# Performance work log

Measured on AMD Instinct MI355X. Metric: run time of the kernel, lower is better.

## Reference

```python
import jax, jax.numpy as jnp
import numpy as np

B, TE, TD, D = 32, 2048, 64, 1024

def setup_inputs() -> dict:
    key = jax.random.key(0)
    k1, k2, k3, k4, k5 = jax.random.split(key, 5)
    return {
        "encoder_outputs": jax.random.normal(k1, (B, TE, D), dtype=jnp.float32),
        "decoder_outputs": jax.random.normal(k2, (B, TD, D), dtype=jnp.float32),
        "W_a": jax.random.normal(k3, (D, D), dtype=jnp.float32) * (1.0 / np.sqrt(D)),
        "U_a": jax.random.normal(k4, (D, D), dtype=jnp.float32) * (1.0 / np.sqrt(D)),
        "V_a": jax.random.normal(k5, (D, 1), dtype=jnp.float32) * (1.0 / np.sqrt(D)),
    }

def reference(encoder_outputs, decoder_outputs, W_a, U_a, V_a):
    # Bahdanau additive attention over encoder positions, query = last decoder step.
    dec_last = decoder_outputs[:, -1, :]                      # [B, D]
    enc_W = jnp.einsum('bte,ef->btf', encoder_outputs, W_a)   # [B, Te, D]
    dec_U = jnp.einsum('bd,df->bf', dec_last, U_a)            # [B, D] (broadcast over Te instead of tile)
    tanh_out = jnp.tanh(enc_W + dec_U[:, None, :])            # [B, Te, D]
    scores = jnp.einsum('btf,fo->bt', tanh_out, V_a[:, 0:1])  # [B, Te] (squeeze of [B,Te,1])
    weights = jax.nn.softmax(scores, axis=1)                  # [B, Te]
    context = jnp.einsum('bte,bt->be', encoder_outputs, weights)  # [B, D]
    return context, weights[..., None]
```

## Files before the change

kernel.cpp:

```cpp
#include <hip/hip_runtime.h>
#include <stdint.h>

typedef __attribute__((ext_vector_type(8))) __bf16 bf16x8;
typedef __attribute__((ext_vector_type(4))) float  f32x4;

__device__ __forceinline__ uint16_t f2b(float f) {
  uint32_t u = __float_as_uint(f);
  u += 0x7fffu + ((u >> 16) & 1u);
  return (uint16_t)(u >> 16);
}
__device__ __forceinline__ float b2f_lo(uint32_t p) { return __uint_as_float(p << 16); }
__device__ __forceinline__ float b2f_hi(uint32_t p) { return __uint_as_float(p & 0xffff0000u); }

__device__ __forceinline__ float tanh_fast(float x) {
  float e = __expf(2.0f * x);
  return 1.0f - 2.0f / (e + 1.0f);
}

__device__ __forceinline__ void bar() { asm volatile("s_barrier" ::: "memory"); }

__device__ __forceinline__ void gload16(const void* g, void* l) {
  __builtin_amdgcn_global_load_lds(
      (__attribute__((address_space(1))) uint32_t*)g,
      (__attribute__((address_space(3))) uint32_t*)l, 16, 0, 0);
}

__global__ __launch_bounds__(256) void convert_enc(const float4* __restrict__ in,
                                                   uint4* __restrict__ out) {
  int i = blockIdx.x * 256 + threadIdx.x;
  float4 a = in[2 * i], b = in[2 * i + 1];
  uint4 o;
  o.x = (uint32_t)f2b(a.x) | ((uint32_t)f2b(a.y) << 16);
  o.y = (uint32_t)f2b(a.z) | ((uint32_t)f2b(a.w) << 16);
  o.z = (uint32_t)f2b(b.x) | ((uint32_t)f2b(b.y) << 16);
  o.w = (uint32_t)f2b(b.z) | ((uint32_t)f2b(b.w) << 16);
  out[i] = o;
}

__global__ __launch_bounds__(256) void convert_WT(const float* __restrict__ W,
                                                  uint16_t* __restrict__ WT) {
  __shared__ float tile[64][65];
  int k0 = (blockIdx.x & 15) * 64;
  int n0 = (blockIdx.x >> 4) * 64;
  #pragma unroll
  for (int it = 0; it < 16; ++it) {
    int idx = it * 256 + threadIdx.x;
    int kr = idx >> 6, nc = idx & 63;
    tile[kr][nc] = W[(size_t)(k0 + kr) * 1024 + n0 + nc];
  }
  __syncthreads();
  #pragma unroll
  for (int it = 0; it < 16; ++it) {
    int idx = it * 256 + threadIdx.x;
    int nr = idx >> 6, kc = idx & 63;
    WT[(size_t)(n0 + nr) * 1024 + k0 + kc] = f2b(tile[kc][nr]);
  }
}

__global__ __launch_bounds__(256) void compute_u(const float* __restrict__ dec,
                                                 const float4* __restrict__ U4,
                                                 float* __restrict__ u) {
  int b = blockIdx.x >> 3, dseg = blockIdx.x & 7;
  __shared__ float sdec[128];
  if (threadIdx.x < 128)
    sdec[threadIdx.x] = dec[(size_t)b * 64 * 1024 + 63 * 1024 + dseg * 128 + threadIdx.x];
  __syncthreads();
  float4 a = {0.f, 0.f, 0.f, 0.f};
  const float4* Ub = U4 + (size_t)dseg * 128 * 256 + threadIdx.x;
  #pragma unroll 4
  for (int d = 0; d < 128; ++d) {
    float4 w = Ub[(size_t)d * 256];
    float s = sdec[d];
    a.x = fmaf(s, w.x, a.x);
    a.y = fmaf(s, w.y, a.y);
    a.z = fmaf(s, w.z, a.z);
    a.w = fmaf(s, w.w, a.w);
  }
  float* up = u + b * 1024 + threadIdx.x * 4;
  atomicAdd(up + 0, a.x);
  atomicAdd(up + 1, a.y);
  atomicAdd(up + 2, a.z);
  atomicAdd(up + 3, a.w);
}

__global__ __launch_bounds__(512, 2) void gemm_score(const uint16_t* __restrict__ A,
                                                     const uint16_t* __restrict__ BT,
                                                     const float* __restrict__ u,
                                                     const float* __restrict__ v,
                                                     float* __restrict__ spart) {
  __shared__ uint4 lds4[4][2][1024];
  __shared__ float sred[4][256];

  const int bx = blockIdx.x;
  const int wg = (bx & 7) * 128 + (bx >> 3);
  const int mtile = wg >> 2;
  const int ntile = wg & 3;

  const int tid = threadIdx.x;
  const int lane = tid & 63;
  const int wid = tid >> 6;
  const int wr = wid >> 2;
  const int wc = wid & 3;
  const int nib = lane & 15;
  const int q4 = lane >> 4;
  const int fx = q4 ^ ((nib >> 1) & 3);

  const int rowA = mtile * 256;
  const char* baseA = (const char*)A + (size_t)rowA * 2048;
  const char* baseB = (const char*)BT + (size_t)ntile * 256 * 2048;
  const size_t srcoff = (size_t)(tid >> 2) * 2048 +
                        ((size_t)((tid & 3) ^ ((tid >> 3) & 3)) << 4);

#define STAGE_OP(buf, op, srcbase, kt)                                        \
  do {                                                                        \
    const char* _s = (const char*)(srcbase) + (size_t)(kt) * 64;              \
    gload16(_s + srcoff,              &lds4[(buf)][(op)][wid * 64]);          \
    gload16(_s + srcoff + 128 * 2048, &lds4[(buf)][(op)][512 + wid * 64]);    \
  } while (0)

  f32x4 acc[8][4];
  #pragma unroll
  for (int i = 0; i < 8; ++i)
    #pragma unroll
    for (int j = 0; j < 4; ++j) acc[i][j] = (f32x4){0.f, 0.f, 0.f, 0.f};

  STAGE_OP(0, 0, baseA, 0); STAGE_OP(0, 1, baseB, 0);
  STAGE_OP(1, 0, baseA, 1); STAGE_OP(1, 1, baseB, 1);
  STAGE_OP(2, 0, baseA, 2); STAGE_OP(2, 1, baseB, 2);
  asm volatile("s_waitcnt vmcnt(8)" ::: "memory");
  bar();

  bf16x8 bfr[4];

#define PHASE(cb_, qi_, ...)                                                  \
  do {                                                                        \
    bf16x8 af[4];                                                             \
    _Pragma("unroll")                                                         \
    for (int i = 0; i < 4; ++i)                                               \
      af[i] = *(const bf16x8*)&lds4[cb_][0]                                   \
              [(wr * 128 + (qi_) * 64 + i * 16 + nib) * 4 + fx];              \
    if ((qi_) == 0) {                                                         \
      _Pragma("unroll")                                                       \
      for (int j = 0; j < 4; ++j)                                             \
        bfr[j] = *(const bf16x8*)&lds4[cb_][1]                                \
                 [(wc * 64 + j * 16 + nib) * 4 + fx];                         \
    }                                                                         \
    __VA_ARGS__;                                                              \
    bar();                                                                    \
    __builtin_amdgcn_s_setprio(1);                                            \
    _Pragma("unroll")                                                         \
    for (int i = 0; i < 4; ++i)                                               \
      _Pragma("unroll")                                                       \
      for (int j = 0; j < 4; ++j)                                             \
        acc[(qi_) * 4 + i][j] = __builtin_amdgcn_mfma_f32_16x16x32_bf16(      \
            af[i], bfr[j], acc[(qi_) * 4 + i][j], 0, 0, 0);                   \
    __builtin_amdgcn_s_setprio(0);                                            \
  } while (0)

  for (int t = 0; t < 32; ++t) {
    const int cb = t & 3, sb = (t + 3) & 3;
    const bool st = (t < 29);
    PHASE(cb, 0, if (st) STAGE_OP(sb, 0, baseA, t + 3));
    bar();
    PHASE(cb, 1, if (st) STAGE_OP(sb, 1, baseB, t + 3));
    if (t < 29)       asm volatile("s_waitcnt vmcnt(8)" ::: "memory");
    else if (t == 29) asm volatile("s_waitcnt vmcnt(4)" ::: "memory");
    else if (t == 30) asm volatile("s_waitcnt vmcnt(0)" ::: "memory");
    bar();
  }
#undef PHASE
#undef STAGE_OP

  const int b = mtile >> 3;
  float vv[4], uu[4];
  #pragma unroll
  for (int j = 0; j < 4; ++j) {
    int col = ntile * 256 + wc * 64 + j * 16 + nib;
    vv[j] = v[col];
    uu[j] = u[b * 1024 + col];
  }
  #pragma unroll
  for (int qi = 0; qi < 2; ++qi)
    #pragma unroll
    for (int i = 0; i < 4; ++i)
      #pragma unroll
      for (int reg = 0; reg < 4; ++reg) {
        float s = 0.f;
        #pragma unroll
        for (int j = 0; j < 4; ++j) s += vv[j] * tanh_fast(acc[qi * 4 + i][j][reg] + uu[j]);
        s += __shfl_xor(s, 1);
        s += __shfl_xor(s, 2);
        s += __shfl_xor(s, 4);
        s += __shfl_xor(s, 8);
        if (nib == 0) sred[wc][wr * 128 + qi * 64 + i * 16 + q4 * 4 + reg] = s;
      }
  __syncthreads();
  if (tid < 256) {
    float s = sred[0][tid] + sred[1][tid] + sred[2][tid] + sred[3][tid];
    spart[(size_t)ntile * 65536 + rowA + tid] = s;
  }
}

__global__ __launch_bounds__(256) void softmax_k(const float* __restrict__ spart,
                                                 float* __restrict__ wout) {
  int b = blockIdx.x, tid = threadIdx.x;
  __shared__ float red[4];
  float sv[8];
  float mx = -1e30f;
  #pragma unroll
  for (int i = 0; i < 8; ++i) {
    int idx = b * 2048 + i * 256 + tid;
    float s = 0.f;
    #pragma unroll
    for (int j = 0; j < 4; ++j) s += spart[j * 65536 + idx];
    sv[i] = s;
    mx = fmaxf(mx, s);
  }
  #pragma unroll
  for (int off = 1; off < 64; off <<= 1) mx = fmaxf(mx, __shfl_xor(mx, off));
  if ((tid & 63) == 0) red[tid >> 6] = mx;
  __syncthreads();
  mx = fmaxf(fmaxf(red[0], red[1]), fmaxf(red[2], red[3]));
  __syncthreads();
  float sum = 0.f;
  #pragma unroll
  for (int i = 0; i < 8; ++i) {
    sv[i] = __expf(sv[i] - mx);
    sum += sv[i];
  }
  #pragma unroll
  for (int off = 1; off < 64; off <<= 1) sum += __shfl_xor(sum, off);
  if ((tid & 63) == 0) red[tid >> 6] = sum;
  __syncthreads();
  float inv = 1.0f / (red[0] + red[1] + red[2] + red[3]);
  #pragma unroll
  for (int i = 0; i < 8; ++i) wout[b * 2048 + i * 256 + tid] = sv[i] * inv;
}

__global__ __launch_bounds__(256) void context_k(const uint16_t* __restrict__ encA,
                                                 const float* __restrict__ w,
                                                 float* __restrict__ ctx) {
  int b = blockIdx.x >> 4, ch = blockIdx.x & 15;
  int t0 = ch * 128;
  __shared__ float lw[128];
  if (threadIdx.x < 128) lw[threadIdx.x] = w[b * 2048 + t0 + threadIdx.x];
  __syncthreads();
  int th = threadIdx.x >> 7;
  int i  = threadIdx.x & 127;
  int e0 = i * 8;
  float a[8] = {0.f, 0.f, 0.f, 0.f, 0.f, 0.f, 0.f, 0.f};
  const uint16_t* base = encA + (size_t)b * 2048 * 1024 + (size_t)(t0 + th * 64) * 1024 + e0;
  const float* lwp = lw + th * 64;
  #pragma unroll 2
  for (int t = 0; t < 64; ++t) {
    uint4 p = *(const uint4*)(base + (size_t)t * 1024);
    float wt = lwp[t];
    a[0] = fmaf(wt, b2f_lo(p.x), a[0]);
    a[1] = fmaf(wt, b2f_hi(p.x), a[1]);
    a[2] = fmaf(wt, b2f_lo(p.y), a[2]);
    a[3] = fmaf(wt, b2f_hi(p.y), a[3]);
    a[4] = fmaf(wt, b2f_lo(p.z), a[4]);
    a[5] = fmaf(wt, b2f_hi(p.z), a[5]);
    a[6] = fmaf(wt, b2f_lo(p.w), a[6]);
    a[7] = fmaf(wt, b2f_hi(p.w), a[7]);
  }
  float* cp = &ctx[b * 1024 + e0];
  #pragma unroll
  for (int k = 0; k < 8; ++k) atomicAdd(cp + k, a[k]);
}

extern "C" void kernel_launch(void* const* d_in, const int* in_sizes, int n_in,
                              void* d_out, int out_size, void* d_ws, size_t ws_size,
                              hipStream_t stream) {
  const float* enc = (const float*)d_in[0];
  const float* dec = (const float*)d_in[1];
  const float* Wa  = (const float*)d_in[2];
  const float* Ua  = (const float*)d_in[3];
  const float* Va  = (const float*)d_in[4];

  float* out = (float*)d_out;
  float* ctx = out;
  float* wts = out + 32 * 1024;

  char* ws = (char*)d_ws;
  uint16_t* encA  = (uint16_t*)ws;
  uint16_t* WT    = (uint16_t*)(ws + 134217728);
  float*    ub    = (float*)  (ws + 136314880);
  float*    spart = (float*)  (ws + 136445952);

  hipMemsetAsync(ctx, 0, 32 * 1024 * sizeof(float), stream);
  hipMemsetAsync(ub, 0, 32 * 1024 * sizeof(float), stream);

  convert_enc<<<32768, 256, 0, stream>>>((const float4*)enc, (uint4*)encA);
  convert_WT<<<256, 256, 0, stream>>>(Wa, WT);
  compute_u<<<256, 256, 0, stream>>>(dec, (const float4*)Ua, ub);
  gemm_score<<<1024, 512, 0, stream>>>(encA, WT, ub, Va, spart);
  softmax_k<<<32, 256, 0, stream>>>(spart, wts);
  context_k<<<512, 256, 0, stream>>>(encA, wts, ctx);
}
```

Measured before the change: 630.5 us.

## Retile score GEMM to 128x128 with B fragments from global, remove atomics in context

The score GEMM moves from 256x256 tiles with 512 threads and a 4-deep LDS pipeline to 128x128 tiles with 256 threads and 128-wide K steps. Only A is staged in a double-buffered, swizzled LDS, while B fragments are loaded straight from global memory into registers and prefetched one step ahead. Scores are now split across 8 N-tiles, so softmax sums 8 partials. The context kernel writes per-chunk partials that a new reduce kernel sums, replacing float atomics and the memset. The smaller tiles raise global traffic for W and give less reuse per block.

```diff
diff --git a/kernel.cpp b/kernel.cpp
--- a/kernel.cpp
+++ b/kernel.cpp
@@ -18,6 +18,7 @@
 }
 
 __device__ __forceinline__ void bar() { asm volatile("s_barrier" ::: "memory"); }
+__device__ __forceinline__ void cfence() { asm volatile("" ::: "memory"); }
 
 __device__ __forceinline__ void gload16(const void* g, void* l) {
   __builtin_amdgcn_global_load_lds(
@@ -83,121 +84,140 @@
   atomicAdd(up + 3, a.w);
 }
 
-__global__ __launch_bounds__(512, 2) void gemm_score(const uint16_t* __restrict__ A,
+__global__ __launch_bounds__(256, 2) void gemm_score(const uint16_t* __restrict__ A,
                                                      const uint16_t* __restrict__ BT,
                                                      const float* __restrict__ u,
                                                      const float* __restrict__ v,
                                                      float* __restrict__ spart) {
-  __shared__ uint4 lds4[4][2][1024];
-  __shared__ float sred[4][256];
+  __shared__ uint4 sA[2][1024];
+  __shared__ float sred[128];
 
   const int bx = blockIdx.x;
-  const int wg = (bx & 7) * 128 + (bx >> 3);
-  const int mtile = wg >> 2;
-  const int ntile = wg & 3;
+  const int wgl = (bx & 7) * 512 + (bx >> 3);
+  const int mtile = wgl >> 3;
+  const int ntile = wgl & 7;
 
   const int tid = threadIdx.x;
   const int lane = tid & 63;
   const int wid = tid >> 6;
-  const int wr = wid >> 2;
-  const int wc = wid & 3;
+  const int wm = (wid >> 1) * 64;
+  const int wn = (wid & 1) * 64;
   const int nib = lane & 15;
   const int q4 = lane >> 4;
-  const int fx = q4 ^ ((nib >> 1) & 3);
-
-  const int rowA = mtile * 256;
+
+  const int rowA = mtile * 128;
   const char* baseA = (const char*)A + (size_t)rowA * 2048;
-  const char* baseB = (const char*)BT + (size_t)ntile * 256 * 2048;
-  const size_t srcoff = (size_t)(tid >> 2) * 2048 +
-                        ((size_t)((tid & 3) ^ ((tid >> 3) & 3)) << 4);
-
-#define STAGE_OP(buf, op, srcbase, kt)                                        \
+  const size_t srcoff = (size_t)(tid >> 3) * 2048 +
+                        ((size_t)((tid & 7) ^ ((tid >> 3) & 7)) << 4);
+  const char* pB = (const char*)BT + (size_t)(ntile * 128 + wn + nib) * 2048 + q4 * 16;
+
+  f32x4 acc[4][4];
+  #pragma unroll
+  for (int i = 0; i < 4; ++i)
+    #pragma unroll
+    for (int j = 0; j < 4; ++j) acc[i][j] = (f32x4){0.f, 0.f, 0.f, 0.f};
+
+  bf16x8 Bn0[4][2], Bn1[4][2];
+
+#define ASTAGE(buf, koff)                                                     \
   do {                                                                        \
-    const char* _s = (const char*)(srcbase) + (size_t)(kt) * 64;              \
-    gload16(_s + srcoff,              &lds4[(buf)][(op)][wid * 64]);          \
-    gload16(_s + srcoff + 128 * 2048, &lds4[(buf)][(op)][512 + wid * 64]);    \
+    _Pragma("unroll")                                                         \
+    for (int s = 0; s < 4; ++s)                                               \
+      gload16(baseA + (koff) + s * 65536 + srcoff,                            \
+              &sA[buf][s * 256 + wid * 64]);                                  \
   } while (0)
 
-  f32x4 acc[8][4];
-  #pragma unroll
-  for (int i = 0; i < 8; ++i)
-    #pragma unroll
-    for (int j = 0; j < 4; ++j) acc[i][j] = (f32x4){0.f, 0.f, 0.f, 0.f};
-
-  STAGE_OP(0, 0, baseA, 0); STAGE_OP(0, 1, baseB, 0);
-  STAGE_OP(1, 0, baseA, 1); STAGE_OP(1, 1, baseB, 1);
-  STAGE_OP(2, 0, baseA, 2); STAGE_OP(2, 1, baseB, 2);
+#define BLOAD(dst, koff)                                                      \
+  do {                                                                        \
+    _Pragma("unroll")                                                         \
+    for (int j = 0; j < 4; ++j)                                               \
+      _Pragma("unroll")                                                       \
+      for (int kk = 0; kk < 2; ++kk)                                          \
+        dst[j][kk] = *(const bf16x8*)(pB + (koff) + j * 32768 + kk * 64);     \
+  } while (0)
+
+  ASTAGE(0, 0);
+  cfence();
+  BLOAD(Bn0, 0);
   asm volatile("s_waitcnt vmcnt(8)" ::: "memory");
   bar();
 
-  bf16x8 bfr[4];
-
-#define PHASE(cb_, qi_, ...)                                                  \
+#define STEP(P, Bcur, Bnxt, t, STG)                                           \
   do {                                                                        \
-    bf16x8 af[4];                                                             \
+    if (STG) ASTAGE(P ^ 1, ((t) + 1) * 128);                                  \
+    cfence();                                                                 \
+    bf16x8 af[4][2];                                                          \
     _Pragma("unroll")                                                         \
-    for (int i = 0; i < 4; ++i)                                               \
-      af[i] = *(const bf16x8*)&lds4[cb_][0]                                   \
-              [(wr * 128 + (qi_) * 64 + i * 16 + nib) * 4 + fx];              \
-    if ((qi_) == 0) {                                                         \
+    for (int mi = 0; mi < 4; ++mi)                                            \
       _Pragma("unroll")                                                       \
-      for (int j = 0; j < 4; ++j)                                             \
-        bfr[j] = *(const bf16x8*)&lds4[cb_][1]                                \
-                 [(wc * 64 + j * 16 + nib) * 4 + fx];                         \
-    }                                                                         \
-    __VA_ARGS__;                                                              \
-    bar();                                                                    \
+      for (int kk = 0; kk < 2; ++kk)                                          \
+        af[mi][kk] = *(const bf16x8*)&sA[P][(wm + mi * 16 + nib) * 8 +        \
+                                           (((kk << 2) + q4) ^ (nib & 7))];   \
+    if (STG) BLOAD(Bnxt, ((t) + 1) * 128);                                    \
     __builtin_amdgcn_s_setprio(1);                                            \
     _Pragma("unroll")                                                         \
-    for (int i = 0; i < 4; ++i)                                               \
+    for (int mi = 0; mi < 4; ++mi)                                            \
       _Pragma("unroll")                                                       \
-      for (int j = 0; j < 4; ++j)                                             \
-        acc[(qi_) * 4 + i][j] = __builtin_amdgcn_mfma_f32_16x16x32_bf16(      \
-            af[i], bfr[j], acc[(qi_) * 4 + i][j], 0, 0, 0);                   \
+      for (int nj = 0; nj < 4; ++nj)                                          \
+        _Pragma("unroll")                                                     \
+        for (int kk = 0; kk < 2; ++kk)                                        \
+          acc[mi][nj] = __builtin_amdgcn_mfma_f32_16x16x32_bf16(              \
+              af[mi][kk], Bcur[nj][kk], acc[mi][nj], 0, 0, 0);                \
     __builtin_amdgcn_s_setprio(0);                                            \
+    if (STG) asm volatile("s_waitcnt vmcnt(8)" ::: "memory");                 \
+    bar();                                                                    \
   } while (0)
 
-  for (int t = 0; t < 32; ++t) {
-    const int cb = t & 3, sb = (t + 3) & 3;
-    const bool st = (t < 29);
-    PHASE(cb, 0, if (st) STAGE_OP(sb, 0, baseA, t + 3));
-    bar();
-    PHASE(cb, 1, if (st) STAGE_OP(sb, 1, baseB, t + 3));
-    if (t < 29)       asm volatile("s_waitcnt vmcnt(8)" ::: "memory");
-    else if (t == 29) asm volatile("s_waitcnt vmcnt(4)" ::: "memory");
-    else if (t == 30) asm volatile("s_waitcnt vmcnt(0)" ::: "memory");
-    bar();
-  }
-#undef PHASE
-#undef STAGE_OP
-
-  const int b = mtile >> 3;
+  #pragma unroll
+  for (int tt = 0; tt < 8; ++tt) {
+    STEP(0, Bn0, Bn1, 2 * tt, true);
+    STEP(1, Bn1, Bn0, 2 * tt + 1, (tt < 7));
+  }
+#undef STEP
+#undef BLOAD
+#undef ASTAGE
+
+  const int b = mtile >> 4;
   float vv[4], uu[4];
   #pragma unroll
   for (int j = 0; j < 4; ++j) {
-    int col = ntile * 256 + wc * 64 + j * 16 + nib;
+    int col = ntile * 128 + wn + j * 16 + nib;
     vv[j] = v[col];
     uu[j] = u[b * 1024 + col];
   }
-  #pragma unroll
-  for (int qi = 0; qi < 2; ++qi)
-    #pragma unroll
-    for (int i = 0; i < 4; ++i)
+  float sloc[4][4];
+  #pragma unroll
+  for (int mi = 0; mi < 4; ++mi)
+    #pragma unroll
+    for (int reg = 0; reg < 4; ++reg) {
+      float s = 0.f;
       #pragma unroll
-      for (int reg = 0; reg < 4; ++reg) {
-        float s = 0.f;
-        #pragma unroll
-        for (int j = 0; j < 4; ++j) s += vv[j] * tanh_fast(acc[qi * 4 + i][j][reg] + uu[j]);
-        s += __shfl_xor(s, 1);
-        s += __shfl_xor(s, 2);
-        s += __shfl_xor(s, 4);
-        s += __shfl_xor(s, 8);
-        if (nib == 0) sred[wc][wr * 128 + qi * 64 + i * 16 + q4 * 4 + reg] = s;
-      }
-  __syncthreads();
-  if (tid < 256) {
-    float s = sred[0][tid] + sred[1][tid] + sred[2][tid] + sred[3][tid];
-    spart[(size_t)ntile * 65536 + rowA + tid] = s;
+      for (int j = 0; j < 4; ++j) s += vv[j] * tanh_fast(acc[mi][j][reg] + uu[j]);
+      s += __shfl_xor(s, 1);
+      s += __shfl_xor(s, 2);
+      s += __shfl_xor(s, 4);
+      s += __shfl_xor(s, 8);
+      sloc[mi][reg] = s;
+    }
+  if ((wid & 1) == 0 && nib == 0) {
+    #pragma unroll
+    for (int mi = 0; mi < 4; ++mi)
+      #pragma unroll
+      for (int reg = 0; reg < 4; ++reg)
+        sred[wm + mi * 16 + q4 * 4 + reg] = sloc[mi][reg];
+  }
+  __syncthreads();
+  if ((wid & 1) == 1 && nib == 0) {
+    float* outp = spart + (size_t)ntile * 65536 + rowA;
+    #pragma unroll
+    for (int mi = 0; mi < 4; ++mi) {
+      int r = wm + mi * 16 + q4 * 4;
+      float4 sv;
+      #pragma unroll
+      for (int reg = 0; reg < 4; ++reg)
+        ((float*)&sv)[reg] = sloc[mi][reg] + sred[r + reg];
+      *(float4*)(outp + r) = sv;
+    }
   }
 }
 
@@ -212,7 +232,7 @@
     int idx = b * 2048 + i * 256 + tid;
     float s = 0.f;
     #pragma unroll
-    for (int j = 0; j < 4; ++j) s += spart[j * 65536 + idx];
+    for (int j = 0; j < 8; ++j) s += spart[j * 65536 + idx];
     sv[i] = s;
     mx = fmaxf(mx, s);
   }
@@ -237,12 +257,13 @@
   for (int i = 0; i < 8; ++i) wout[b * 2048 + i * 256 + tid] = sv[i] * inv;
 }
 
-__global__ __launch_bounds__(256) void context_k(const uint16_t* __restrict__ encA,
-                                                 const float* __restrict__ w,
-                                                 float* __restrict__ ctx) {
+__global__ __launch_bounds__(256) void context_part(const uint16_t* __restrict__ encA,
+                                                    const float* __restrict__ w,
+                                                    float* __restrict__ cpart) {
   int b = blockIdx.x >> 4, ch = blockIdx.x & 15;
   int t0 = ch * 128;
   __shared__ float lw[128];
+  __shared__ float sctx[1024];
   if (threadIdx.x < 128) lw[threadIdx.x] = w[b * 2048 + t0 + threadIdx.x];
   __syncthreads();
   int th = threadIdx.x >> 7;
@@ -264,9 +285,31 @@
     a[6] = fmaf(wt, b2f_lo(p.w), a[6]);
     a[7] = fmaf(wt, b2f_hi(p.w), a[7]);
   }
-  float* cp = &ctx[b * 1024 + e0];
-  #pragma unroll
-  for (int k = 0; k < 8; ++k) atomicAdd(cp + k, a[k]);
+  if (th == 0) {
+    #pragma unroll
+    for (int k = 0; k < 8; ++k) sctx[e0 + k] = a[k];
+  }
+  __syncthreads();
+  if (th == 1) {
+    float* cp = cpart + (size_t)(b * 16 + ch) * 1024 + e0;
+    float4 v0, v1;
+    #pragma unroll
+    for (int k = 0; k < 4; ++k) ((float*)&v0)[k] = a[k] + sctx[e0 + k];
+    #pragma unroll
+    for (int k = 0; k < 4; ++k) ((float*)&v1)[k] = a[4 + k] + sctx[e0 + 4 + k];
+    *(float4*)(cp) = v0;
+    *(float4*)(cp + 4) = v1;
+  }
+}
+
+__global__ __launch_bounds__(256) void ctx_reduce(const float* __restrict__ cpart,
+                                                  float* __restrict__ ctx) {
+  int idx = blockIdx.x * 256 + threadIdx.x;
+  int b = idx >> 10, e = idx & 1023;
+  float s = 0.f;
+  #pragma unroll
+  for (int r = 0; r < 16; ++r) s += cpart[(size_t)(b * 16 + r) * 1024 + e];
+  ctx[idx] = s;
 }
 
 extern "C" void kernel_launch(void* const* d_in, const int* in_sizes, int n_in,
@@ -287,14 +330,15 @@
   uint16_t* WT    = (uint16_t*)(ws + 134217728);
   float*    ub    = (float*)  (ws + 136314880);
   float*    spart = (float*)  (ws + 136445952);
-
-  hipMemsetAsync(ctx, 0, 32 * 1024 * sizeof(float), stream);
+  float*    cpart = spart;
+
   hipMemsetAsync(ub, 0, 32 * 1024 * sizeof(float), stream);
 
   convert_enc<<<32768, 256, 0, stream>>>((const float4*)enc, (uint4*)encA);
   convert_WT<<<256, 256, 0, stream>>>(Wa, WT);
   compute_u<<<256, 256, 0, stream>>>(dec, (const float4*)Ua, ub);
-  gemm_score<<<1024, 512, 0, stream>>>(encA, WT, ub, Va, spart);
+  gemm_score<<<4096, 256, 0, stream>>>(encA, WT, ub, Va, spart);
   softmax_k<<<32, 256, 0, stream>>>(spart, wts);
-  context_k<<<512, 256, 0, stream>>>(encA, wts, ctx);
-}
+  context_part<<<512, 256, 0, stream>>>(encA, wts, cpart);
+  ctx_reduce<<<128, 256, 0, stream>>>(cpart, ctx);
+}
```

After: 724.0 us. 14.8% more time.
